# Kernel tuning notes

Measured on AMD Instinct MI355X. Metric: run time of the kernel, lower is better.

Reference implementation:

```python
import jax, jax.numpy as jnp
import numpy as np

T = 40          # self.T / timestep
T_REDUCE = 32
FAC = T_REDUCE / T - 0.001  # 0.799, threshold used by create_spike_input_cuda


def conv_t(x, w, b, pad):
    # x: (N,C,H,W,T); w: (O,I,3,3). SLAYER/catSNN conv = Conv3d with time-kernel 1,
    # i.e. the same 2D conv applied independently at every timestep.
    out = jax.lax.conv_general_dilated(
        x, w[..., None], window_strides=(1, 1, 1),
        padding=[(pad, pad), (pad, pad), (0, 0)],
        dimension_numbers=("NCHWT", "OIHWT", "NCHWT"))
    return out + b[None, :, None, None, None]


def avgpool2(x):
    # 2x2 spatial average pool per timestep (snn.pool(2))
    N, C, H, W, Tt = x.shape
    return x.reshape(N, C, H // 2, 2, W // 2, 2, Tt).mean(axis=(3, 5))


def get_spikes(x, thr):
    # catCuda.getSpikes: integrate-and-fire over the last (time) axis with
    # soft reset (subtract threshold). thr broadcastable to x[..., 0].
    xT = jnp.moveaxis(x, -1, 0)                      # (T, N, C, H, W)
    thr_b = jnp.broadcast_to(jnp.asarray(thr, x.dtype), xT.shape[1:])
    def step(v, xt):
        v = v + xt
        s = (v >= thr_b).astype(x.dtype)
        return v - s * thr_b, s
    _, s = jax.lax.scan(step, jnp.zeros(xT.shape[1:], x.dtype), xT)
    return jnp.moveaxis(s, 0, -1)


def requant(y):
    # create_spike_input_cuda(sum(y, time)/T, T): stack the time-mean T times
    # and spike-generate with threshold FAC.
    ym = jnp.mean(y, axis=-1)                        # sum over time / T
    yb = jnp.broadcast_to(ym[..., None], ym.shape + (T,))
    return get_spikes(yb, FAC)


def tts(xi, yi, thr):
    # threshold_training_snn: per-channel spiking of xi, requantized copy of yi.
    return get_spikes(xi, thr[None, :, None, None]), requant(yi)


def forward(x, thr1, thr2, thr3, thr4, thr5, thr6, thr7, p1, p2, p3, p4,
            w1, b1, w2, b2, w3, b3, w4, b4, w5, b5, w6, b6, w7, b7, wc, bc):
    c = conv_t(x, w1, b1, 1)
    xs, ys = tts(c, c, thr1)
    xs, ys = tts(conv_t(xs, w2, b2, 1), conv_t(ys, w2, b2, 1), thr2)
    xs, ys = tts(avgpool2(xs), avgpool2(ys), p1)
    xs, ys = tts(conv_t(xs, w3, b3, 1), conv_t(ys, w3, b3, 1), thr3)
    xs, ys = tts(conv_t(xs, w4, b4, 1), conv_t(ys, w4, b4, 1), thr4)
    xs, ys = tts(avgpool2(xs), avgpool2(ys), p2)
    xs, ys = tts(conv_t(xs, w5, b5, 1), conv_t(ys, w5, b5, 1), thr5)
    xs, ys = tts(conv_t(xs, w6, b6, 1), conv_t(ys, w6, b6, 1), thr6)
    xs, ys = tts(avgpool2(xs), avgpool2(ys), p3)
    xs, ys = tts(conv_t(xs, w7, b7, 0), conv_t(ys, w7, b7, 0), thr7)
    xs, ys = tts(avgpool2(xs), avgpool2(ys), p4)
    N = xs.shape[0]
    xr = xs.reshape(N, 1024, T)                      # spatial is 1x1 here
    logits = jnp.einsum("nct,oc->not", xr, wc) + bc[None, :, None]
    out = jnp.sum(logits, axis=-1) / T               # sum_spikes / T
    return out.reshape(N, 10, 1, 1)


def setup_inputs() -> dict:
    key = jax.random.key(0)
    ks = jax.random.split(key, 32)
    inp = {}
    inp["x"] = jax.random.uniform(ks[0], (2, 3, 32, 32, T), jnp.float32)
    chans = [(3, 128), (128, 128), (128, 256), (256, 256),
             (256, 512), (512, 512), (512, 1024)]
    for i, (ci, co) in enumerate(chans, 1):
        inp[f"w{i}"] = jax.random.normal(ks[i], (co, ci, 3, 3), jnp.float32) * (2.0 / (ci * 9)) ** 0.5
        inp[f"b{i}"] = jnp.zeros((co,), jnp.float32)
    inp["wc"] = jax.random.normal(ks[8], (10, 1024), jnp.float32) * 0.03
    inp["bc"] = jnp.zeros((10,), jnp.float32)
    thr_dims = {"thr1": 128, "thr2": 128, "p1": 128, "thr3": 256, "thr4": 256,
                "p2": 256, "thr5": 512, "thr6": 512, "p3": 512, "thr7": 1024, "p4": 1024}
    for j, (name, d) in enumerate(thr_dims.items()):
        inp[name] = 0.2 + jax.random.uniform(ks[9 + j], (d,), jnp.float32)
    return inp


def reference(x, thr1, thr2, thr3, thr4, thr5, thr6, thr7, p1, p2, p3, p4,
              w1, b1, w2, b2, w3, b3, w4, b4, w5, b5, w6, b6, w7, b7, wc, bc):
    return forward(x, thr1, thr2, thr3, thr4, thr5, thr6, thr7, p1, p2, p3, p4,
                   w1, b1, w2, b2, w3, b3, w4, b4, w5, b5, w6, b6, w7, b7, wc, bc)
```

## Files before the change

kernel.cpp:

```cpp
#include <hip/hip_runtime.h>


constexpr int NT = 40;

typedef __attribute__((ext_vector_type(8))) short s16x8;
typedef __attribute__((ext_vector_type(4))) float f32x4;

__device__ __forceinline__ float bf2f(unsigned short u) {
    return __uint_as_float(((unsigned)u) << 16);
}

__device__ __forceinline__ void wg_barrier() {
    __builtin_amdgcn_sched_barrier(0);
    __builtin_amdgcn_s_barrier();
    __builtin_amdgcn_sched_barrier(0);
}

__global__ __launch_bounds__(256) void transpose_w(
    const float* __restrict__ w, float* __restrict__ wt, int CO, int R)
{
    __shared__ float tile[32][33];
    const int r0 = blockIdx.x * 32, c0 = blockIdx.y * 32;
    const int tx = threadIdx.x % 32, ty = threadIdx.x / 32;
#pragma unroll
    for (int k = 0; k < 4; k++) {
        const int co = c0 + ty + k * 8, r = r0 + tx;
        if (co < CO && r < R) tile[ty + k * 8][tx] = w[(size_t)co * R + r];
    }
    __syncthreads();
#pragma unroll
    for (int k = 0; k < 4; k++) {
        const int r = r0 + ty + k * 8, co = c0 + tx;
        if (r < R && co < CO) wt[(size_t)r * CO + co] = tile[tx][ty + k * 8];
    }
}

__global__ __launch_bounds__(320) void conv1_c(
    const float* __restrict__ in, const float* __restrict__ wt,
    const float* __restrict__ bias, float* __restrict__ out)
{
    __shared__ float xs_[27 * NT];
    __shared__ float wl[27 * 128];
    const int sp = blockIdx.x;
    const int ho = sp >> 5, wo = sp & 31;
    const int n = blockIdx.z;
    const int tid = threadIdx.x;
    const int tt = tid >> 5;
    const int cc = tid & 31;

    float4 acc[4];
#pragma unroll
    for (int j = 0; j < 4; j++) {
        const float bv = bias[cc * 4 + j];
        acc[j] = make_float4(bv, bv, bv, bv);
    }
    for (int u = tid; u < 270; u += 320) {
        const int r = u / 10, q = u % 10;
        const int cil = r / 9, k = r % 9;
        const int hi = ho + k / 3 - 1, wi = wo + k % 3 - 1;
        float4 v = make_float4(0.f, 0.f, 0.f, 0.f);
        if ((unsigned)hi < 32u && (unsigned)wi < 32u)
            v = *reinterpret_cast<const float4*>(
                in + ((size_t)((n * 3 + cil) * 1024 + hi * 32 + wi)) * NT + q * 4);
        *reinterpret_cast<float4*>(&xs_[r * NT + q * 4]) = v;
    }
    for (int u = tid; u < 864; u += 320) {
        const int r = u >> 5, j = u & 31;
        *reinterpret_cast<float4*>(&wl[r * 128 + j * 4]) =
            *reinterpret_cast<const float4*>(wt + r * 128 + j * 4);
    }
    __syncthreads();
#pragma unroll
    for (int r = 0; r < 27; ++r) {
        const float4 xv = *reinterpret_cast<const float4*>(&xs_[r * NT + tt * 4]);
        const float4 wv = *reinterpret_cast<const float4*>(&wl[r * 128 + cc * 4]);
        acc[0].x = fmaf(xv.x, wv.x, acc[0].x); acc[0].y = fmaf(xv.y, wv.x, acc[0].y);
        acc[0].z = fmaf(xv.z, wv.x, acc[0].z); acc[0].w = fmaf(xv.w, wv.x, acc[0].w);
        acc[1].x = fmaf(xv.x, wv.y, acc[1].x); acc[1].y = fmaf(xv.y, wv.y, acc[1].y);
        acc[1].z = fmaf(xv.z, wv.y, acc[1].z); acc[1].w = fmaf(xv.w, wv.y, acc[1].w);
        acc[2].x = fmaf(xv.x, wv.z, acc[2].x); acc[2].y = fmaf(xv.y, wv.z, acc[2].y);
        acc[2].z = fmaf(xv.z, wv.z, acc[2].z); acc[2].w = fmaf(xv.w, wv.z, acc[2].w);
        acc[3].x = fmaf(xv.x, wv.w, acc[3].x); acc[3].y = fmaf(xv.y, wv.w, acc[3].y);
        acc[3].z = fmaf(xv.z, wv.w, acc[3].z); acc[3].w = fmaf(xv.w, wv.w, acc[3].w);
    }
    const size_t base = (size_t)(n * 1024 + sp) * (NT * 128);
#pragma unroll
    for (int j = 0; j < 4; j++) {
        const int cb = cc * 4 + j;
        out[base + (tt * 4 + 0) * 128 + cb] = acc[j].x;
        out[base + (tt * 4 + 1) * 128 + cb] = acc[j].y;
        out[base + (tt * 4 + 2) * 128 + cb] = acc[j].z;
        out[base + (tt * 4 + 3) * 128 + cb] = acc[j].w;
    }
}

__global__ void split_w(const float* __restrict__ w,
                        unsigned short* __restrict__ hi, unsigned short* __restrict__ mid,
                        unsigned short* __restrict__ lo, int CO, int CIN_)
{
    const int idx = blockIdx.x * blockDim.x + threadIdx.x;
    if (idx >= CO * CIN_) return;
    const int co = idx / CIN_, ci = idx % CIN_;
    const float* src = w + ((size_t)co * CIN_ + ci) * 9;
#pragma unroll
    for (int k = 0; k < 9; ++k) {
        const float f = src[k];
        const unsigned u = __float_as_uint(f);
        const float fh = __uint_as_float(u & 0xFFFF0000u);
        const float r1 = f - fh;
        const unsigned u1 = __float_as_uint(r1);
        const float fm = __uint_as_float(u1 & 0xFFFF0000u);
        const float r2 = r1 - fm;
        const unsigned u2 = __float_as_uint(r2);
        const size_t dst = ((size_t)k * CO + co) * CIN_ + ci;
        hi[dst] = (unsigned short)(u >> 16);
        mid[dst] = (unsigned short)(u1 >> 16);
        lo[dst] = (unsigned short)(u2 >> 16);
    }
}

template<int CIN_SEG, int COUT, int HP, int WP, int NSPLIT>
__global__ __launch_bounds__(256, 2) void conv_t14(
    const unsigned short* __restrict__ spk,
    const unsigned short* __restrict__ wlo, const unsigned short* __restrict__ wmid,
    const unsigned short* __restrict__ whi,
    const float* __restrict__ bias, float* __restrict__ out)
{
    constexpr int CIN = CIN_SEG * NSPLIT;
    constexpr int HO = HP - 2, WO = WP - 2;
    constexpr int MROW = WO * NT;
    constexpr int MTILES = (MROW + 63) / 64;
    constexpr int KC = CIN_SEG / 64;
    constexpr int NCHUNK = 9 * KC;
    static_assert(NCHUNK % 2 == 0, "chunk loop unrolled by 2");
    constexpr int NX = HO * MTILES;
    constexpr int NY = COUT / 64;
    constexpr int NB = NX * NSPLIT * NY;
    static_assert(NB % 8 == 0, "grid must divide across 8 XCDs");
    constexpr int Q = NB / 8;
    constexpr size_t SLAB = (size_t)2 * HO * WO * NT * COUT;

    __shared__ unsigned short smem[20480];

    const int g = blockIdx.x;
    const int orig = (g & 7) * Q + (g >> 3);
    const int x = orig % NX;
    const int split = (orig / NX) % NSPLIT;
    const int y = orig / (NX * NSPLIT);
    const int ho = x / MTILES;
    const int m0 = (x % MTILES) * 64;
    const int co0 = y * 64;

    const int tid = threadIdx.x;
    const int lane = tid & 63;
    const int wv = tid >> 6;
    const int wm = wv >> 1, wn = wv & 1;
    const int lr = lane >> 4, lc = lane & 15;
    const int rlane = lane >> 3, blane = lane & 7;
    const int swz = ((blane ^ rlane) << 3);

    int lofs[10]; int arow[10]; int gstat[10]; const unsigned short* wbase[10]; bool isA[10];
#pragma unroll
    for (int s = 0; s < 10; ++s) {
        const int slot = wv * 10 + s;
        if (slot < 16) {
            const int img = slot >> 3, r0 = (slot & 7) << 3;
            isA[s] = true;
            arow[s] = m0 + r0 + rlane;
            lofs[s] = (img * 64 + r0 + rlane) * 64 + swz;
            gstat[s] = (int)((img * HP * WP * NT + arow[s]) * CIN + blane * 8);
            wbase[s] = spk;
        } else {
            const int si = slot - 16;
            const int sp_ = si >> 3, r0 = (si & 7) << 3;
            isA[s] = false;
            arow[s] = 0;
            lofs[s] = 8192 + (sp_ * 64 + r0 + rlane) * 64 + swz;
            gstat[s] = (int)((co0 + r0 + rlane) * CIN + blane * 8);
            wbase[s] = (sp_ == 0) ? wlo : ((sp_ == 1) ? wmid : whi);
        }
    }

    f32x4 acc[2][2][2];
#pragma unroll
    for (int img = 0; img < 2; ++img)
#pragma unroll
        for (int mf = 0; mf < 2; ++mf)
#pragma unroll
            for (int nf = 0; nf < 2; ++nf) {
                const float bv = (NSPLIT == 1 || split == 0)
                    ? bias[co0 + wn * 32 + nf * 16 + lc] : 0.f;
                acc[img][mf][nf] = {bv, bv, bv, bv};
            }

    auto loadchunk = [&](s16x8 (&r)[10], int c) {
        const int kh = c / (3 * KC);
        const int rem = c - kh * 3 * KC;
        const int kw = rem / KC;
        const int kc = rem - kw * KC;
        const int khw = kh * 3 + kw;
        const int ci0 = split * CIN_SEG + kc * 64;
        const size_t aoff = ((size_t)(ho + kh) * WP * NT + (size_t)kw * NT) * CIN + ci0;
        const size_t boff = (size_t)khw * COUT * CIN + ci0;
#pragma unroll
        for (int s = 0; s < 10; ++s) {
            if (isA[s]) {
                s16x8 v = {0, 0, 0, 0, 0, 0, 0, 0};
                if (arow[s] < MROW)
                    v = *(const s16x8*)(spk + aoff + (size_t)gstat[s]);
                r[s] = v;
            } else {
                r[s] = *(const s16x8*)(wbase[s] + boff + (size_t)gstat[s]);
            }
        }
    };

    auto writechunk = [&](s16x8 (&r)[10]) {
#pragma unroll
        for (int s = 0; s < 10; ++s)
            *(s16x8*)&smem[lofs[s]] = r[s];
    };

    auto compute = [&]() {
#pragma unroll
        for (int kcs = 0; kcs < 2; ++kcs) {
            const int cswz = (((kcs * 4 + lr) ^ (lc & 7)) << 3);
            s16x8 af[2][2];
#pragma unroll
            for (int img = 0; img < 2; ++img)
#pragma unroll
                for (int mf = 0; mf < 2; ++mf)
                    af[img][mf] = *(const s16x8*)&smem[(img * 64 + wm * 32 + mf * 16 + lc) * 64 + cswz];
#pragma unroll
            for (int s = 0; s < 3; ++s)
#pragma unroll
                for (int nf = 0; nf < 2; ++nf) {
                    const s16x8 bq = *(const s16x8*)&smem[8192 + s * 4096 + (wn * 32 + nf * 16 + lc) * 64 + cswz];
#pragma unroll
                    for (int img = 0; img < 2; ++img)
#pragma unroll
                        for (int mf = 0; mf < 2; ++mf)
                            acc[img][mf][nf] = __builtin_amdgcn_mfma_f32_16x16x32_bf16(
                                af[img][mf], bq, acc[img][mf][nf], 0, 0, 0);
                }
        }
    };

    s16x8 ra[10], rb[10];
    loadchunk(ra, 0);
#pragma unroll 1
    for (int c = 0; c < NCHUNK; c += 2) {
        writechunk(ra);
        loadchunk(rb, c + 1);
        asm volatile("s_waitcnt lgkmcnt(0)" ::: "memory");
        wg_barrier();
        compute();
        wg_barrier();
        writechunk(rb);
        if (c + 2 < NCHUNK) loadchunk(ra, c + 2);
        asm volatile("s_waitcnt lgkmcnt(0)" ::: "memory");
        wg_barrier();
        compute();
        wg_barrier();
    }

#pragma unroll
    for (int img = 0; img < 2; ++img) {
        float* outp = out + (size_t)split * SLAB + ((size_t)(img * HO + ho) * WO * NT) * COUT;
#pragma unroll
        for (int mf = 0; mf < 2; ++mf) {
            const int mbase = m0 + wm * 32 + mf * 16;
            if (mbase >= MROW) continue;
#pragma unroll
            for (int nf = 0; nf < 2; ++nf) {
                const int col = co0 + wn * 32 + nf * 16 + lc;
#pragma unroll
                for (int j = 0; j < 4; ++j) {
                    const int m = mbase + lr * 4 + j;
                    outp[(size_t)m * COUT + col] = acc[img][mf][nf][j];
                }
            }
        }
    }
}

__global__ void halo_zero(unsigned short* __restrict__ buf, int HP, int WP, int TC)
{
    const int cell = blockIdx.x, n = blockIdx.y;
    int h, w;
    if (cell < WP)            { h = 0;       w = cell; }
    else if (cell < 2 * WP)   { h = HP - 1;  w = cell - WP; }
    else { const int s = cell - 2 * WP; h = 1 + (s >> 1); w = (s & 1) ? (WP - 1) : 0; }
    unsigned short* p = buf + (((size_t)(n * HP + h) * WP) + w) * TC;
    const s16x8 z = {0, 0, 0, 0, 0, 0, 0, 0};
    for (int i = threadIdx.x * 8; i < TC; i += blockDim.x * 8)
        *(s16x8*)(p + i) = z;
}

__global__ void if_ci(const float* __restrict__ in, unsigned short* __restrict__ spk,
                      const float* __restrict__ thr, int C, int HO, int WO,
                      int HP, int WP, int off, int total)
{
    const int idx = blockIdx.x * blockDim.x + threadIdx.x;
    if (idx >= total) return;
    const int c = idx % C;
    const int sp = idx / C;
    const int wo = sp % WO;
    const int ho = (sp / WO) % HO;
    const int n = sp / (WO * HO);
    const float th = thr[c];
    const size_t ib = (size_t)sp * NT * C + c;
    const size_t ob = (((size_t)(n * HP + ho + off) * WP) + wo + off) * NT * C + c;
    float v = 0.f;
#pragma unroll
    for (int t = 0; t < NT; ++t) {
        v += in[ib + (size_t)t * C];
        const float s = (v >= th) ? 1.f : 0.f;
        v -= s * th;
        spk[ob + (size_t)t * C] = (s != 0.f) ? (unsigned short)0x3F80 : (unsigned short)0;
    }
}

__global__ void pool_ci(const unsigned short* __restrict__ in, unsigned short* __restrict__ out,
                        const float* __restrict__ thr, int C, int HO, int WO,
                        int IHP, int IWP, int offi, int OHP, int OWP, int offo, int total)
{
    const int idx = blockIdx.x * blockDim.x + threadIdx.x;
    if (idx >= total) return;
    const int c = idx % C;
    const int sp = idx / C;
    const int wo = sp % WO;
    const int ho = (sp / WO) % HO;
    const int n = sp / (WO * HO);
    const float th = thr[c];
    const size_t i00 = (((size_t)(n * IHP + 2 * ho + offi) * IWP) + 2 * wo + offi) * NT * C + c;
    const size_t dW = (size_t)NT * C, dH = (size_t)IWP * NT * C;
    const size_t ob = (((size_t)(n * OHP + ho + offo) * OWP) + wo + offo) * NT * C + c;
    float v = 0.f;
#pragma unroll
    for (int t = 0; t < NT; ++t) {
        const size_t o = (size_t)t * C;
        const float a = bf2f(in[i00 + o]) + bf2f(in[i00 + dW + o]) +
                        bf2f(in[i00 + dH + o]) + bf2f(in[i00 + dH + dW + o]);
        v += a * 0.25f;
        const float s = (v >= th) ? 1.f : 0.f;
        v -= s * th;
        out[ob + o] = (s != 0.f) ? (unsigned short)0x3F80 : (unsigned short)0;
    }
}

__global__ void reduce_if7(const float* __restrict__ part, unsigned short* __restrict__ out,
                           const float* __restrict__ thr, int total)
{
    const int idx = blockIdx.x * blockDim.x + threadIdx.x;
    if (idx >= total) return;
    const int c = idx & 1023;
    const size_t base = (size_t)(idx >> 10) * NT * 1024 + c;
    const size_t SL = 327680;
    const float th = thr[c];
    float v = 0.f;
#pragma unroll
    for (int t = 0; t < NT; ++t) {
        const size_t o = (size_t)t * 1024;
        const float x = part[base + o] + part[SL + base + o] +
                        part[2 * SL + base + o] + part[3 * SL + base + o];
        v += x;
        const float s = (v >= th) ? 1.f : 0.f;
        v -= s * th;
        out[base + o] = (s != 0.f) ? (unsigned short)0x3F80 : (unsigned short)0;
    }
}

__global__ __launch_bounds__(1024) void classifier_ci(
    const unsigned short* __restrict__ s, const float* __restrict__ wc,
    const float* __restrict__ bc, float* __restrict__ out)
{
    __shared__ float cnt[2][1024];
    const int c = threadIdx.x;
    for (int n = 0; n < 2; n++) {
        float sum = 0.f;
#pragma unroll
        for (int t = 0; t < NT; ++t) sum += bf2f(s[(size_t)(n * NT + t) * 1024 + c]);
        cnt[n][c] = sum;
    }
    __syncthreads();
    if (threadIdx.x < 20) {
        const int n = threadIdx.x / 10, o = threadIdx.x % 10;
        float a = 0.f;
        for (int k = 0; k < 1024; k++) a += cnt[n][k] * wc[o * 1024 + k];
        out[n * 10 + o] = a * (1.f / 40.f) + bc[o];
    }
}

extern "C" void kernel_launch(void* const* d_in, const int* in_sizes, int n_in,
                              void* d_out, int out_size, void* d_ws, size_t ws_size,
                              hipStream_t stream)
{
    const float* x   = (const float*)d_in[0];
    const float* w1  = (const float*)d_in[1];  const float* b1 = (const float*)d_in[2];
    const float* w2  = (const float*)d_in[3];  const float* b2 = (const float*)d_in[4];
    const float* w3  = (const float*)d_in[5];  const float* b3 = (const float*)d_in[6];
    const float* w4  = (const float*)d_in[7];  const float* b4 = (const float*)d_in[8];
    const float* w5  = (const float*)d_in[9];  const float* b5 = (const float*)d_in[10];
    const float* w6  = (const float*)d_in[11]; const float* b6 = (const float*)d_in[12];
    const float* w7  = (const float*)d_in[13]; const float* b7 = (const float*)d_in[14];
    const float* wc  = (const float*)d_in[15]; const float* bc = (const float*)d_in[16];
    const float* thr1 = (const float*)d_in[17];
    const float* thr2 = (const float*)d_in[18];
    const float* p1   = (const float*)d_in[19];
    const float* thr3 = (const float*)d_in[20];
    const float* thr4 = (const float*)d_in[21];
    const float* p2   = (const float*)d_in[22];
    const float* thr5 = (const float*)d_in[23];
    const float* thr6 = (const float*)d_in[24];
    const float* p3   = (const float*)d_in[25];
    const float* thr7 = (const float*)d_in[26];
    const float* p4   = (const float*)d_in[27];

    char* W0 = (char*)d_ws;
    float* OUT = (float*)W0;
    unsigned short* WH   = (unsigned short*)(W0 + (40ull << 20));
    unsigned short* WMID = (unsigned short*)(W0 + (49ull << 20));
    unsigned short* WLO  = (unsigned short*)(W0 + (58ull << 20));
    unsigned short* R1   = (unsigned short*)(W0 + (67ull << 20));
    unsigned short* R2   = (unsigned short*)(W0 + (90ull << 20));
    unsigned short* R3   = (unsigned short*)(W0 + (97ull << 20));
    float* WT1 = (float*)(W0 + (117ull << 20));
    unsigned short* S1 = R1, *S3 = R1, *S5 = R1;
    unsigned short* S2 = R2, *S4 = R2, *S6 = R2;
    unsigned short* U2 = R3, *U4 = R3, *U6 = R3;
    unsigned short* S7 = R3;
    unsigned short* P4 = (unsigned short*)((char*)R3 + (2ull << 20));
    float* O = (float*)d_out;

    transpose_w<<<dim3(1, 4), 256, 0, stream>>>(w1, WT1, 128, 27);
    conv1_c<<<dim3(1024, 1, 2), 320, 0, stream>>>(x, WT1, b1, OUT);
    halo_zero<<<dim3(132, 2), 256, 0, stream>>>(S1, 34, 34, 5120);
    if_ci<<<1024, 256, 0, stream>>>(OUT, S1, thr1, 128, 32, 32, 34, 34, 1, 262144);

    split_w<<<64, 256, 0, stream>>>(w2, WH, WMID, WLO, 128, 128);
    conv_t14<128, 128, 34, 34, 1><<<1280, 256, 0, stream>>>(S1, WLO, WMID, WH, b2, OUT);
    if_ci<<<1024, 256, 0, stream>>>(OUT, U2, thr2, 128, 32, 32, 32, 32, 0, 262144);
    halo_zero<<<dim3(68, 2), 256, 0, stream>>>(S2, 18, 18, 5120);
    pool_ci<<<256, 256, 0, stream>>>(U2, S2, p1, 128, 16, 16, 32, 32, 0, 18, 18, 1, 65536);

    split_w<<<128, 256, 0, stream>>>(w3, WH, WMID, WLO, 256, 128);
    conv_t14<128, 256, 18, 18, 1><<<640, 256, 0, stream>>>(S2, WLO, WMID, WH, b3, OUT);
    halo_zero<<<dim3(68, 2), 256, 0, stream>>>(S3, 18, 18, 10240);
    if_ci<<<512, 256, 0, stream>>>(OUT, S3, thr3, 256, 16, 16, 18, 18, 1, 131072);

    split_w<<<256, 256, 0, stream>>>(w4, WH, WMID, WLO, 256, 256);
    conv_t14<256, 256, 18, 18, 1><<<640, 256, 0, stream>>>(S3, WLO, WMID, WH, b4, OUT);
    if_ci<<<512, 256, 0, stream>>>(OUT, U4, thr4, 256, 16, 16, 16, 16, 0, 131072);
    halo_zero<<<dim3(36, 2), 256, 0, stream>>>(S4, 10, 10, 10240);
    pool_ci<<<128, 256, 0, stream>>>(U4, S4, p2, 256, 8, 8, 16, 16, 0, 10, 10, 1, 32768);

    split_w<<<512, 256, 0, stream>>>(w5, WH, WMID, WLO, 512, 256);
    conv_t14<256, 512, 10, 10, 1><<<320, 256, 0, stream>>>(S4, WLO, WMID, WH, b5, OUT);
    halo_zero<<<dim3(36, 2), 256, 0, stream>>>(S5, 10, 10, 20480);
    if_ci<<<256, 256, 0, stream>>>(OUT, S5, thr5, 512, 8, 8, 10, 10, 1, 65536);

    split_w<<<1024, 256, 0, stream>>>(w6, WH, WMID, WLO, 512, 512);
    conv_t14<512, 512, 10, 10, 1><<<320, 256, 0, stream>>>(S5, WLO, WMID, WH, b6, OUT);
    if_ci<<<256, 256, 0, stream>>>(OUT, U6, thr6, 512, 8, 8, 8, 8, 0, 65536);
    pool_ci<<<64, 256, 0, stream>>>(U6, S6, p3, 512, 4, 4, 8, 8, 0, 4, 4, 0, 16384);

    split_w<<<2048, 256, 0, stream>>>(w7, WH, WMID, WLO, 1024, 512);
    conv_t14<128, 1024, 4, 4, 4><<<256, 256, 0, stream>>>(S6, WLO, WMID, WH, b7, OUT);
    reduce_if7<<<32, 256, 0, stream>>>(OUT, S7, thr7, 8192);
    pool_ci<<<8, 256, 0, stream>>>(S7, P4, p4, 1024, 1, 1, 2, 2, 0, 1, 1, 0, 2048);

    classifier_ci<<<1, 1024, 0, stream>>>(P4, wc, bc, O);
}
```

Baseline: 623.6 us.

## Triple-buffer conv chunks, split-K deep layers, fuse halo zeroing into IF kernels

The conv kernel's software pipeline moves from double to triple register buffering, raises wave priority during MFMA compute, and skips bounds checks when the row tiles divide evenly. Layers 5–7 now use split-K over input channels (NSPLIT 2/2/8) to put more blocks on the GPU, and the generic IF kernel sums the partial slabs, replacing the dedicated reduce kernel. Halo zeroing is folded into the IF and pool kernels as extra blocks, removing separate launches. The costs are higher register pressure from the third buffer, extra partial-sum traffic through a larger workspace, and a non-unrolled time loop in the IF kernel.

```diff
diff --git a/kernel.cpp b/kernel.cpp
--- a/kernel.cpp
+++ b/kernel.cpp
@@ -130,12 +130,13 @@
     constexpr int HO = HP - 2, WO = WP - 2;
     constexpr int MROW = WO * NT;
     constexpr int MTILES = (MROW + 63) / 64;
+    constexpr bool RAGGED = (MROW % 64) != 0;
     constexpr int KC = CIN_SEG / 64;
     constexpr int NCHUNK = 9 * KC;
-    static_assert(NCHUNK % 2 == 0, "chunk loop unrolled by 2");
+    static_assert(NCHUNK % 3 == 0, "rotation unrolled by 3");
     constexpr int NX = HO * MTILES;
     constexpr int NY = COUT / 64;
-    constexpr int NB = NX * NSPLIT * NY;
+    constexpr int NB = NX * NY * NSPLIT;
     static_assert(NB % 8 == 0, "grid must divide across 8 XCDs");
     constexpr int Q = NB / 8;
     constexpr size_t SLAB = (size_t)2 * HO * WO * NT * COUT;
@@ -145,8 +146,8 @@
     const int g = blockIdx.x;
     const int orig = (g & 7) * Q + (g >> 3);
     const int x = orig % NX;
-    const int split = (orig / NX) % NSPLIT;
-    const int y = orig / (NX * NSPLIT);
+    const int y = (orig / NX) % NY;
+    const int split = orig / (NX * NY);
     const int ho = x / MTILES;
     const int m0 = (x % MTILES) * 64;
     const int co0 = y * 64;
@@ -205,10 +206,14 @@
 #pragma unroll
         for (int s = 0; s < 10; ++s) {
             if (isA[s]) {
-                s16x8 v = {0, 0, 0, 0, 0, 0, 0, 0};
-                if (arow[s] < MROW)
-                    v = *(const s16x8*)(spk + aoff + (size_t)gstat[s]);
-                r[s] = v;
+                if (!RAGGED) {
+                    r[s] = *(const s16x8*)(spk + aoff + (size_t)gstat[s]);
+                } else {
+                    s16x8 v = {0, 0, 0, 0, 0, 0, 0, 0};
+                    if (arow[s] < MROW)
+                        v = *(const s16x8*)(spk + aoff + (size_t)gstat[s]);
+                    r[s] = v;
+                }
             } else {
                 r[s] = *(const s16x8*)(wbase[s] + boff + (size_t)gstat[s]);
             }
@@ -222,6 +227,7 @@
     };
 
     auto compute = [&]() {
+        __builtin_amdgcn_s_setprio(1);
 #pragma unroll
         for (int kcs = 0; kcs < 2; ++kcs) {
             const int cswz = (((kcs * 4 + lr) ^ (lc & 7)) << 3);
@@ -244,20 +250,28 @@
                                 af[img][mf], bq, acc[img][mf][nf], 0, 0, 0);
                 }
         }
+        __builtin_amdgcn_s_setprio(0);
     };
 
-    s16x8 ra[10], rb[10];
+    s16x8 ra[10], rb[10], rc[10];
     loadchunk(ra, 0);
+    loadchunk(rb, 1);
 #pragma unroll 1
-    for (int c = 0; c < NCHUNK; c += 2) {
+    for (int c = 0; c < NCHUNK; c += 3) {
         writechunk(ra);
-        loadchunk(rb, c + 1);
+        if (c + 2 < NCHUNK) loadchunk(rc, c + 2);
         asm volatile("s_waitcnt lgkmcnt(0)" ::: "memory");
         wg_barrier();
         compute();
         wg_barrier();
         writechunk(rb);
-        if (c + 2 < NCHUNK) loadchunk(ra, c + 2);
+        if (c + 3 < NCHUNK) loadchunk(ra, c + 3);
+        asm volatile("s_waitcnt lgkmcnt(0)" ::: "memory");
+        wg_barrier();
+        compute();
+        wg_barrier();
+        writechunk(rc);
+        if (c + 4 < NCHUNK) loadchunk(rb, c + 4);
         asm volatile("s_waitcnt lgkmcnt(0)" ::: "memory");
         wg_barrier();
         compute();
@@ -270,7 +284,7 @@
 #pragma unroll
         for (int mf = 0; mf < 2; ++mf) {
             const int mbase = m0 + wm * 32 + mf * 16;
-            if (mbase >= MROW) continue;
+            if (RAGGED && mbase >= MROW) continue;
 #pragma unroll
             for (int nf = 0; nf < 2; ++nf) {
                 const int col = co0 + wn * 32 + nf * 16 + lc;
@@ -284,23 +298,24 @@
     }
 }
 
-__global__ void halo_zero(unsigned short* __restrict__ buf, int HP, int WP, int TC)
-{
-    const int cell = blockIdx.x, n = blockIdx.y;
-    int h, w;
-    if (cell < WP)            { h = 0;       w = cell; }
-    else if (cell < 2 * WP)   { h = HP - 1;  w = cell - WP; }
-    else { const int s = cell - 2 * WP; h = 1 + (s >> 1); w = (s & 1) ? (WP - 1) : 0; }
-    unsigned short* p = buf + (((size_t)(n * HP + h) * WP) + w) * TC;
-    const s16x8 z = {0, 0, 0, 0, 0, 0, 0, 0};
-    for (int i = threadIdx.x * 8; i < TC; i += blockDim.x * 8)
-        *(s16x8*)(p + i) = z;
-}
-
 __global__ void if_ci(const float* __restrict__ in, unsigned short* __restrict__ spk,
                       const float* __restrict__ thr, int C, int HO, int WO,
-                      int HP, int WP, int off, int total)
-{
+                      int HP, int WP, int off, int total, int nslab, size_t slab,
+                      int nmain, int halocells)
+{
+    if ((int)blockIdx.x >= nmain) {
+        const int hb = blockIdx.x - nmain;
+        const int n = hb / halocells, cell = hb % halocells;
+        int h, w;
+        if (cell < WP)          { h = 0;      w = cell; }
+        else if (cell < 2 * WP) { h = HP - 1; w = cell - WP; }
+        else { const int s = cell - 2 * WP; h = 1 + (s >> 1); w = (s & 1) ? (WP - 1) : 0; }
+        unsigned short* p = spk + (((size_t)(n * HP + h) * WP) + w) * (size_t)(NT * C);
+        const s16x8 z = {0, 0, 0, 0, 0, 0, 0, 0};
+        for (int i = threadIdx.x * 8; i < NT * C; i += blockDim.x * 8)
+            *(s16x8*)(p + i) = z;
+        return;
+    }
     const int idx = blockIdx.x * blockDim.x + threadIdx.x;
     if (idx >= total) return;
     const int c = idx % C;
@@ -312,9 +327,11 @@
     const size_t ib = (size_t)sp * NT * C + c;
     const size_t ob = (((size_t)(n * HP + ho + off) * WP) + wo + off) * NT * C + c;
     float v = 0.f;
-#pragma unroll
+#pragma unroll 1
     for (int t = 0; t < NT; ++t) {
-        v += in[ib + (size_t)t * C];
+        float x = 0.f;
+        for (int s = 0; s < nslab; ++s) x += in[ib + (size_t)s * slab + (size_t)t * C];
+        v += x;
         const float s = (v >= th) ? 1.f : 0.f;
         v -= s * th;
         spk[ob + (size_t)t * C] = (s != 0.f) ? (unsigned short)0x3F80 : (unsigned short)0;
@@ -323,8 +340,22 @@
 
 __global__ void pool_ci(const unsigned short* __restrict__ in, unsigned short* __restrict__ out,
                         const float* __restrict__ thr, int C, int HO, int WO,
-                        int IHP, int IWP, int offi, int OHP, int OWP, int offo, int total)
-{
+                        int IHP, int IWP, int offi, int OHP, int OWP, int offo,
+                        int total, int nmain, int halocells)
+{
+    if ((int)blockIdx.x >= nmain) {
+        const int hb = blockIdx.x - nmain;
+        const int n = hb / halocells, cell = hb % halocells;
+        int h, w;
+        if (cell < OWP)          { h = 0;       w = cell; }
+        else if (cell < 2 * OWP) { h = OHP - 1; w = cell - OWP; }
+        else { const int s = cell - 2 * OWP; h = 1 + (s >> 1); w = (s & 1) ? (OWP - 1) : 0; }
+        unsigned short* p = out + (((size_t)(n * OHP + h) * OWP) + w) * (size_t)(NT * C);
+        const s16x8 z = {0, 0, 0, 0, 0, 0, 0, 0};
+        for (int i = threadIdx.x * 8; i < NT * C; i += blockDim.x * 8)
+            *(s16x8*)(p + i) = z;
+        return;
+    }
     const int idx = blockIdx.x * blockDim.x + threadIdx.x;
     if (idx >= total) return;
     const int c = idx % C;
@@ -346,28 +377,6 @@
         const float s = (v >= th) ? 1.f : 0.f;
         v -= s * th;
         out[ob + o] = (s != 0.f) ? (unsigned short)0x3F80 : (unsigned short)0;
-    }
-}
-
-__global__ void reduce_if7(const float* __restrict__ part, unsigned short* __restrict__ out,
-                           const float* __restrict__ thr, int total)
-{
-    const int idx = blockIdx.x * blockDim.x + threadIdx.x;
-    if (idx >= total) return;
-    const int c = idx & 1023;
-    const size_t base = (size_t)(idx >> 10) * NT * 1024 + c;
-    const size_t SL = 327680;
-    const float th = thr[c];
-    float v = 0.f;
-#pragma unroll
-    for (int t = 0; t < NT; ++t) {
-        const size_t o = (size_t)t * 1024;
-        const float x = part[base + o] + part[SL + base + o] +
-                        part[2 * SL + base + o] + part[3 * SL + base + o];
-        v += x;
-        const float s = (v >= th) ? 1.f : 0.f;
-        v -= s * th;
-        out[base + o] = (s != 0.f) ? (unsigned short)0x3F80 : (unsigned short)0;
     }
 }
 
@@ -419,13 +428,13 @@
 
     char* W0 = (char*)d_ws;
     float* OUT = (float*)W0;
-    unsigned short* WH   = (unsigned short*)(W0 + (40ull << 20));
-    unsigned short* WMID = (unsigned short*)(W0 + (49ull << 20));
-    unsigned short* WLO  = (unsigned short*)(W0 + (58ull << 20));
-    unsigned short* R1   = (unsigned short*)(W0 + (67ull << 20));
-    unsigned short* R2   = (unsigned short*)(W0 + (90ull << 20));
-    unsigned short* R3   = (unsigned short*)(W0 + (97ull << 20));
-    float* WT1 = (float*)(W0 + (117ull << 20));
+    unsigned short* WH   = (unsigned short*)(W0 + (44ull << 20));
+    unsigned short* WMID = (unsigned short*)(W0 + (53ull << 20));
+    unsigned short* WLO  = (unsigned short*)(W0 + (62ull << 20));
+    unsigned short* R1   = (unsigned short*)(W0 + (71ull << 20));
+    unsigned short* R2   = (unsigned short*)(W0 + (95ull << 20));
+    unsigned short* R3   = (unsigned short*)(W0 + (102ull << 20));
+    float* WT1 = (float*)(W0 + (122ull << 20));
     unsigned short* S1 = R1, *S3 = R1, *S5 = R1;
     unsigned short* S2 = R2, *S4 = R2, *S6 = R2;
     unsigned short* U2 = R3, *U4 = R3, *U6 = R3;
@@ -435,40 +444,46 @@
 
     transpose_w<<<dim3(1, 4), 256, 0, stream>>>(w1, WT1, 128, 27);
     conv1_c<<<dim3(1024, 1, 2), 320, 0, stream>>>(x, WT1, b1, OUT);
-    halo_zero<<<dim3(132, 2), 256, 0, stream>>>(S1, 34, 34, 5120);
-    if_ci<<<1024, 256, 0, stream>>>(OUT, S1, thr1, 128, 32, 32, 34, 34, 1, 262144);
+    if_ci<<<1024 + 264, 256, 0, stream>>>(OUT, S1, thr1, 128, 32, 32, 34, 34, 1,
+                                          262144, 1, 0, 1024, 132);
 
     split_w<<<64, 256, 0, stream>>>(w2, WH, WMID, WLO, 128, 128);
     conv_t14<128, 128, 34, 34, 1><<<1280, 256, 0, stream>>>(S1, WLO, WMID, WH, b2, OUT);
-    if_ci<<<1024, 256, 0, stream>>>(OUT, U2, thr2, 128, 32, 32, 32, 32, 0, 262144);
-    halo_zero<<<dim3(68, 2), 256, 0, stream>>>(S2, 18, 18, 5120);
-    pool_ci<<<256, 256, 0, stream>>>(U2, S2, p1, 128, 16, 16, 32, 32, 0, 18, 18, 1, 65536);
+    if_ci<<<1024, 256, 0, stream>>>(OUT, U2, thr2, 128, 32, 32, 32, 32, 0,
+                                    262144, 1, 0, 1024, 0);
+    pool_ci<<<256 + 136, 256, 0, stream>>>(U2, S2, p1, 128, 16, 16, 32, 32, 0,
+                                           18, 18, 1, 65536, 256, 68);
 
     split_w<<<128, 256, 0, stream>>>(w3, WH, WMID, WLO, 256, 128);
     conv_t14<128, 256, 18, 18, 1><<<640, 256, 0, stream>>>(S2, WLO, WMID, WH, b3, OUT);
-    halo_zero<<<dim3(68, 2), 256, 0, stream>>>(S3, 18, 18, 10240);
-    if_ci<<<512, 256, 0, stream>>>(OUT, S3, thr3, 256, 16, 16, 18, 18, 1, 131072);
+    if_ci<<<512 + 136, 256, 0, stream>>>(OUT, S3, thr3, 256, 16, 16, 18, 18, 1,
+                                         131072, 1, 0, 512, 68);
 
     split_w<<<256, 256, 0, stream>>>(w4, WH, WMID, WLO, 256, 256);
     conv_t14<256, 256, 18, 18, 1><<<640, 256, 0, stream>>>(S3, WLO, WMID, WH, b4, OUT);
-    if_ci<<<512, 256, 0, stream>>>(OUT, U4, thr4, 256, 16, 16, 16, 16, 0, 131072);
-    halo_zero<<<dim3(36, 2), 256, 0, stream>>>(S4, 10, 10, 10240);
-    pool_ci<<<128, 256, 0, stream>>>(U4, S4, p2, 256, 8, 8, 16, 16, 0, 10, 10, 1, 32768);
+    if_ci<<<512, 256, 0, stream>>>(OUT, U4, thr4, 256, 16, 16, 16, 16, 0,
+                                   131072, 1, 0, 512, 0);
+    pool_ci<<<128 + 72, 256, 0, stream>>>(U4, S4, p2, 256, 8, 8, 16, 16, 0,
+                                          10, 10, 1, 32768, 128, 36);
 
     split_w<<<512, 256, 0, stream>>>(w5, WH, WMID, WLO, 512, 256);
-    conv_t14<256, 512, 10, 10, 1><<<320, 256, 0, stream>>>(S4, WLO, WMID, WH, b5, OUT);
-    halo_zero<<<dim3(36, 2), 256, 0, stream>>>(S5, 10, 10, 20480);
-    if_ci<<<256, 256, 0, stream>>>(OUT, S5, thr5, 512, 8, 8, 10, 10, 1, 65536);
+    conv_t14<128, 512, 10, 10, 2><<<640, 256, 0, stream>>>(S4, WLO, WMID, WH, b5, OUT);
+    if_ci<<<256 + 72, 256, 0, stream>>>(OUT, S5, thr5, 512, 8, 8, 10, 10, 1,
+                                        65536, 2, 2621440, 256, 36);
 
     split_w<<<1024, 256, 0, stream>>>(w6, WH, WMID, WLO, 512, 512);
-    conv_t14<512, 512, 10, 10, 1><<<320, 256, 0, stream>>>(S5, WLO, WMID, WH, b6, OUT);
-    if_ci<<<256, 256, 0, stream>>>(OUT, U6, thr6, 512, 8, 8, 8, 8, 0, 65536);
-    pool_ci<<<64, 256, 0, stream>>>(U6, S6, p3, 512, 4, 4, 8, 8, 0, 4, 4, 0, 16384);
+    conv_t14<256, 512, 10, 10, 2><<<640, 256, 0, stream>>>(S5, WLO, WMID, WH, b6, OUT);
+    if_ci<<<256, 256, 0, stream>>>(OUT, U6, thr6, 512, 8, 8, 8, 8, 0,
+                                   65536, 2, 2621440, 256, 0);
+    pool_ci<<<64, 256, 0, stream>>>(U6, S6, p3, 512, 4, 4, 8, 8, 0, 4, 4, 0,
+                                    16384, 64, 0);
 
     split_w<<<2048, 256, 0, stream>>>(w7, WH, WMID, WLO, 1024, 512);
-    conv_t14<128, 1024, 4, 4, 4><<<256, 256, 0, stream>>>(S6, WLO, WMID, WH, b7, OUT);
-    reduce_if7<<<32, 256, 0, stream>>>(OUT, S7, thr7, 8192);
-    pool_ci<<<8, 256, 0, stream>>>(S7, P4, p4, 1024, 1, 1, 2, 2, 0, 1, 1, 0, 2048);
+    conv_t14<64, 1024, 4, 4, 8><<<512, 256, 0, stream>>>(S6, WLO, WMID, WH, b7, OUT);
+    if_ci<<<32, 256, 0, stream>>>(OUT, S7, thr7, 1024, 2, 2, 2, 2, 0,
+                                  8192, 8, 327680, 32, 0);
+    pool_ci<<<8, 256, 0, stream>>>(S7, P4, p4, 1024, 1, 1, 2, 2, 0, 1, 1, 0,
+                                   2048, 8, 0);
 
     classifier_ci<<<1, 1024, 0, stream>>>(P4, wc, bc, O);
 }
```

New measurement: 659.7 us. +5.8%, slower.
